# Kernel optimization log

Measured on AMD Instinct MI355X. Metric: run time of the kernel, lower is better.

## Reference

```python
import jax, jax.numpy as jnp
import numpy as np
import math

B, N, L = 1, 256, 384
D_MSA, D_PAIR, H, DH = 256, 128, 8, 32


def layer_norm(x, g, b, eps=1e-5):
    m = jnp.mean(x, axis=-1, keepdims=True)
    v = jnp.var(x, axis=-1, keepdims=True)
    return (x - m) * jax.lax.rsqrt(v + eps) * g + b


def setup_inputs() -> dict:
    key = jax.random.key(0)
    ks = jax.random.split(key, 16)
    hd = H * DH
    w = lambda k, shp, s=0.05: (jax.random.normal(k, shp, dtype=jnp.float32) * s)
    return {
        "msa": jax.random.normal(ks[0], (B, N, L, D_MSA), dtype=jnp.float32),
        "pair": jax.random.normal(ks[1], (B, L, L, D_PAIR), dtype=jnp.float32),
        "ln_msa_g": jnp.ones((D_MSA,), jnp.float32),
        "ln_msa_b": jnp.zeros((D_MSA,), jnp.float32),
        "ln_pair_g": jnp.ones((D_PAIR,), jnp.float32),
        "ln_pair_b": jnp.zeros((D_PAIR,), jnp.float32),
        "sw_q_w": w(ks[2], (D_MSA, hd)),
        "sw_q_b": jnp.zeros((hd,), jnp.float32),
        "sw_k_w": w(ks[3], (D_MSA, hd)),
        "sw_k_b": jnp.zeros((hd,), jnp.float32),
        "wq": w(ks[4], (D_MSA, hd)),
        "wk": w(ks[5], (D_MSA, hd)),
        "wv": w(ks[6], (D_MSA, hd)),
        "wb": w(ks[7], (D_PAIR, H)),
        "wg": w(ks[8], (D_MSA, hd)),
        "bg": jnp.ones((hd,), jnp.float32),
        "wo": w(ks[9], (hd, D_MSA)),
        "bo": jnp.zeros((D_MSA,), jnp.float32),
    }


def reference(msa, pair, ln_msa_g, ln_msa_b, ln_pair_g, ln_pair_b,
              sw_q_w, sw_q_b, sw_k_w, sw_k_b,
              wq, wk, wv, wb, wg, bg, wo, bo):
    b, n, l, _ = msa.shape
    scale = 1.0 / math.sqrt(DH)

    msa_n = layer_norm(msa, ln_msa_g, ln_msa_b)
    pair_n = layer_norm(pair, ln_pair_g, ln_pair_b)

    # SequenceWeight: attention of target seq (row 0) over all N rows, per (L, head)
    tar = msa_n[:, 0]                                       # [B,L,D]
    swq = (tar @ sw_q_w + sw_q_b).reshape(b, l, H, DH) * scale
    swk = (msa_n @ sw_k_w + sw_k_b).reshape(b, n, l, H, DH)
    sw_logits = jnp.einsum('blhd,bnlhd->bnlh', swq, swk)    # [B,N,L,H]
    seq_weight = jax.nn.softmax(sw_logits, axis=1)          # softmax over N (dropout: eval)

    query = (msa_n @ wq).reshape(b, n, l, H, DH) * seq_weight[..., None]
    key = (msa_n @ wk).reshape(b, n, l, H, DH) * scale
    value = (msa_n @ wv).reshape(b, n, l, H, DH)
    bias = pair_n @ wb                                      # [B,L,L,H]
    gate = jax.nn.sigmoid(msa_n @ wg + bg)                  # [B,N,L,H*DH]

    attn = jnp.einsum('bsqhd,bskhd->bqkh', query, key) + bias
    attn = jax.nn.softmax(attn, axis=-2)                    # over k axis
    out = jnp.einsum('bqkh,bskhd->bsqhd', attn, value).reshape(b, n, l, H * DH)
    out = gate * out
    return out @ wo + bo
```

## Files before the change

### kernel.cpp

```cpp
#include <hip/hip_runtime.h>
#include <hip/hip_fp16.h>
#include <stdint.h>

#define NSEQ 256
#define LSEQ 384
#define DM   256
#define DP   128
#define NH   8
#define DHD  32
#define NL   (NSEQ*LSEQ)
#define LL   (LSEQ*LSEQ)
#define SCALE 0.17677669529663687f

typedef unsigned short u16;
typedef short bf16x8 __attribute__((ext_vector_type(8)));
typedef float f32x4 __attribute__((ext_vector_type(4)));

__device__ __forceinline__ float b2f(u16 s){
  union { uint32_t u; float f; } v; v.u = ((uint32_t)s)<<16; return v.f;
}
__device__ __forceinline__ u16 f2b(float f){
  union { float f; uint32_t u; } v; v.f = f;
  uint32_t u = v.u;
  return (u16)((u + 0x7FFFu + ((u>>16)&1u)) >> 16);
}
__device__ __forceinline__ float wsum(float x){
  #pragma unroll
  for(int o=32;o>0;o>>=1) x += __shfl_xor(x,o,64);
  return x;
}
__device__ __forceinline__ float wmax(float x){
  #pragma unroll
  for(int o=32;o>0;o>>=1) x = fmaxf(x, __shfl_xor(x,o,64));
  return x;
}
__device__ __forceinline__ void gload16(const void* g, void* l){
  __builtin_amdgcn_global_load_lds((const __attribute__((address_space(1))) void*)g,
      (__attribute__((address_space(3))) void*)l, 16, 0, 0);
}

__global__ __launch_bounds__(256) void k_ln_msa(const float* __restrict__ msa,
    const float* __restrict__ g, const float* __restrict__ b, u16* __restrict__ out){
  int lane = threadIdx.x & 63;
  int64_t row = (int64_t)blockIdx.x*4 + (threadIdx.x>>6);
  const float4 x = *(const float4*)(msa + row*DM + lane*4);
  float s = x.x+x.y+x.z+x.w;
  float q = x.x*x.x+x.y*x.y+x.z*x.z+x.w*x.w;
  s = wsum(s); q = wsum(q);
  float mean = s*(1.0f/DM);
  float rstd = rsqrtf(q*(1.0f/DM) - mean*mean + 1e-5f);
  int c = lane*4;
  float4 gv = *(const float4*)(g+c);
  float4 bv = *(const float4*)(b+c);
  ushort4 o;
  o.x=f2b((x.x-mean)*rstd*gv.x+bv.x);
  o.y=f2b((x.y-mean)*rstd*gv.y+bv.y);
  o.z=f2b((x.z-mean)*rstd*gv.z+bv.z);
  o.w=f2b((x.w-mean)*rstd*gv.w+bv.w);
  *(ushort4*)(out + row*DM + c) = o;
}

__global__ __launch_bounds__(256) void k_wconv(const float* __restrict__ wq,
    const float* __restrict__ wk, const float* __restrict__ wv,
    const float* __restrict__ wg, const float* __restrict__ wo,
    u16* __restrict__ WTall, u16* __restrict__ WOT){
  __shared__ float tile[64][65];
  int z = blockIdx.z;
  const float* src = (z==0)?wq:(z==1)?wk:(z==2)?wv:(z==3)?wg:wo;
  u16* dst = (z<4) ? (WTall + z*DM*DM) : WOT;
  int k0 = blockIdx.x*64, n0 = blockIdx.y*64, t = threadIdx.x;
  int r = t>>4, c4 = (t&15)*4;
  #pragma unroll
  for(int it=0; it<4; it++){
    float4 v = *(const float4*)(src + (int64_t)(k0 + it*16 + r)*DM + n0 + c4);
    tile[it*16+r][c4+0]=v.x; tile[it*16+r][c4+1]=v.y;
    tile[it*16+r][c4+2]=v.z; tile[it*16+r][c4+3]=v.w;
  }
  __syncthreads();
  #pragma unroll
  for(int it=0; it<4; it++){
    int nl = it*16 + r, kl = c4;
    ushort4 o;
    o.x=f2b(tile[kl+0][nl]); o.y=f2b(tile[kl+1][nl]);
    o.z=f2b(tile[kl+2][nl]); o.w=f2b(tile[kl+3][nl]);
    *(ushort4*)(dst + (int64_t)(n0+nl)*DM + k0 + kl) = o;
  }
}

__global__ __launch_bounds__(256) void k_u(const u16* __restrict__ msa_n,
    const float* __restrict__ sw_q_w, const float* __restrict__ sw_q_b,
    const float* __restrict__ sw_k_w, float* __restrict__ u){
  __shared__ float tar[DM];
  __shared__ float swq[DM];
  int l = blockIdx.x, t = threadIdx.x;
  tar[t] = b2f(msa_n[(int64_t)l*DM + t]);
  __syncthreads();
  float acc = sw_q_b[t];
  for(int c=0;c<DM;c++) acc += tar[c]*sw_q_w[c*DM + t];
  swq[t] = acc * SCALE;
  __syncthreads();
  float res[NH];
  #pragma unroll
  for(int h=0;h<NH;h++){
    float a = 0.f;
    #pragma unroll
    for(int d=0;d<DHD;d+=4){
      float4 w = *(const float4*)(sw_k_w + t*DM + h*DHD + d);
      a += w.x*swq[h*DHD+d] + w.y*swq[h*DHD+d+1] + w.z*swq[h*DHD+d+2] + w.w*swq[h*DHD+d+3];
    }
    res[h]=a;
  }
  #pragma unroll
  for(int h=0;h<NH;h++) u[((int64_t)l*NH + h)*DM + t] = res[h];
}

__global__ __launch_bounds__(256) void k_seqw(const u16* __restrict__ msa_n,
    const float* __restrict__ u, float* __restrict__ sw){
  __shared__ float ul[NH*DM];
  __shared__ float lg[NH*256];
  __shared__ float mx[NH], sm[NH];
  int l = blockIdx.x, t = threadIdx.x;
  #pragma unroll
  for(int h=0;h<NH;h++) ul[h*DM+t] = u[((int64_t)l*NH+h)*DM + t];
  __syncthreads();
  float acc[NH] = {};
  const u16* row = msa_n + ((int64_t)t*LSEQ + l)*DM;
  for(int c=0;c<DM;c+=4){
    ushort4 xv = *(const ushort4*)(row + c);
    float x0=b2f(xv.x), x1=b2f(xv.y), x2=b2f(xv.z), x3=b2f(xv.w);
    #pragma unroll
    for(int h=0;h<NH;h++)
      acc[h] += x0*ul[h*DM+c] + x1*ul[h*DM+c+1] + x2*ul[h*DM+c+2] + x3*ul[h*DM+c+3];
  }
  #pragma unroll
  for(int h=0;h<NH;h++) lg[h*256+t] = acc[h];
  __syncthreads();
  int wv = t>>6, ln = t&63;
  for(int h=wv; h<NH; h+=4){
    float a=lg[h*256+ln], b=lg[h*256+ln+64], c=lg[h*256+ln+128], d=lg[h*256+ln+192];
    float m = wmax(fmaxf(fmaxf(a,b),fmaxf(c,d)));
    float e = __expf(a-m)+__expf(b-m)+__expf(c-m)+__expf(d-m);
    e = wsum(e);
    if(ln==0){ mx[h]=m; sm[h]=1.f/e; }
  }
  __syncthreads();
  float o[NH];
  #pragma unroll
  for(int h=0;h<NH;h++) o[h] = __expf(acc[h]-mx[h])*sm[h];
  float* dst = sw + ((int64_t)t*LSEQ + l)*NH;
  *(float4*)dst     = make_float4(o[0],o[1],o[2],o[3]);
  *(float4*)(dst+4) = make_float4(o[4],o[5],o[6],o[7]);
}

__global__ __launch_bounds__(256) void k_bias(const float* __restrict__ pair,
    const float* __restrict__ g, const float* __restrict__ b,
    const float* __restrict__ wb, float* __restrict__ bias){
  int64_t row = (int64_t)blockIdx.x*256 + threadIdx.x;
  const float* pr = pair + row*DP;
  uint2 xs[32];
  float s = 0.f, q = 0.f;
  #pragma unroll
  for(int i=0;i<32;i++){
    float4 v = *(const float4*)(pr + i*4);
    s += v.x+v.y+v.z+v.w;
    q += v.x*v.x+v.y*v.y+v.z*v.z+v.w*v.w;
    __half2 p0 = __floats2half2_rn(v.x, v.y);
    __half2 p1 = __floats2half2_rn(v.z, v.w);
    xs[i].x = *(const uint32_t*)&p0;
    xs[i].y = *(const uint32_t*)&p1;
  }
  float mean = s*(1.f/DP);
  float rstd = rsqrtf(q*(1.f/DP) - mean*mean + 1e-5f);
  float acc[NH] = {};
  #pragma unroll
  for(int i=0;i<32;i++){
    __half2 p0 = *(const __half2*)&xs[i].x;
    __half2 p1 = *(const __half2*)&xs[i].y;
    float2 f0 = __half22float2(p0);
    float2 f1 = __half22float2(p1);
    float xv[4] = {f0.x, f0.y, f1.x, f1.y};
    #pragma unroll
    for(int c4=0;c4<4;c4++){
      int c = i*4 + c4;
      float y = (xv[c4]-mean)*rstd*g[c] + b[c];
      #pragma unroll
      for(int h=0;h<NH;h++) acc[h] += y*wb[c*NH+h];
    }
  }
  #pragma unroll
  for(int h=0;h<NH;h++) bias[(int64_t)h*LL + row] = acc[h];
}


__global__ __launch_bounds__(256) void k_projf(const u16* __restrict__ A,
    const u16* __restrict__ WT, u16* __restrict__ qb, u16* __restrict__ kb,
    u16* __restrict__ gbuf, u16* __restrict__ VT,
    const float* __restrict__ sw, const float* __restrict__ bg){
  __shared__ short As[128*256];
  int t = threadIdx.x;
  int w = t>>6, lane = t&63, ln15 = lane&15, quad = lane>>4;
  int mw = (w>>1)*64, nw = (w&1)*64;
  int bx = blockIdx.x;
  int64_t r0 = (int64_t)bx*128;

  {
    int rowl = lane>>5;
    int pc = lane&31;
    #pragma unroll
    for(int m=0;m<16;m++){
      int q = w*16+m;
      int row = 2*q + rowl;
      int gch = pc ^ (row&7);
      gload16(A + (r0+row)*DM + gch*8, &As[q*512]);
    }
  }
  __syncthreads();

  for(int nt=0; nt<8; nt++){
    int n0 = nt*128;
    f32x4 acc[4][4] = {};
    #pragma unroll
    for(int ks=0; ks<8; ks++){
      bf16x8 af[4], bfv[4];
      #pragma unroll
      for(int j=0;j<4;j++)
        bfv[j] = *(const bf16x8*)(WT + (int64_t)(n0+nw+j*16+ln15)*DM + ks*32 + quad*8);
      #pragma unroll
      for(int i=0;i<4;i++){
        int row = mw+i*16+ln15;
        af[i] = *(const bf16x8*)&As[row*256 + (((ks*4+quad) ^ (ln15&7)))*8];
      }
      #pragma unroll
      for(int i=0;i<4;i++)
        #pragma unroll
        for(int j=0;j<4;j++)
          acc[i][j] = __builtin_amdgcn_mfma_f32_16x16x32_bf16(af[i], bfv[j], acc[i][j], 0,0,0);
    }
    int mode = nt>>1;
    int cmb = (nt&1)*128 + nw;
    if(mode==2){
      int s = bx/3, kb3 = (bx%3)*128 + mw;
      #pragma unroll
      for(int j=0;j<4;j++){
        int cm = cmb + j*16 + ln15;
        int hh = cm>>5, d = cm&31;
        #pragma unroll
        for(int i=0;i<4;i++){
          int kpos0 = kb3 + i*16 + quad*4;
          ushort4 o;
          o.x=f2b(acc[i][j][0]); o.y=f2b(acc[i][j][1]);
          o.z=f2b(acc[i][j][2]); o.w=f2b(acc[i][j][3]);
          *(ushort4*)(VT + ((int64_t)(hh*NSEQ+s)*DHD + d)*LSEQ + kpos0) = o;
        }
      }
    } else {
      u16* dst = (mode==0)?qb:(mode==1)?kb:gbuf;
      float bgv[4];
      if(mode==3){
        #pragma unroll
        for(int j=0;j<4;j++) bgv[j] = bg[cmb + j*16 + ln15];
      }
      #pragma unroll
      for(int i=0;i<4;i++)
        #pragma unroll
        for(int reg=0;reg<4;reg++){
          int64_t rr = r0 + mw + i*16 + quad*4 + reg;
          #pragma unroll
          for(int j=0;j<4;j++){
            int cm = cmb + j*16 + ln15;
            float v = acc[i][j][reg];
            if(mode==0)      v *= sw[rr*NH + (cm>>5)];
            else if(mode==1) v *= SCALE;
            else             v = 1.f/(1.f+__expf(-(v+bgv[j])));
            dst[rr*DM + cm] = f2b(v);
          }
        }
    }
  }
}

__global__ __launch_bounds__(256) void k_scores(const u16* __restrict__ Q,
    const u16* __restrict__ K, float* __restrict__ scores){
  __shared__ short As[128*64];
  __shared__ short Bs[128*64];
  int t = threadIdx.x;
  int w = t>>6, lane = t&63, ln15 = lane&15, quad = lane>>4;
  int rIn = lane>>3, cch = lane&7;
  int mw = (w>>1)*64, nw = (w&1)*64;
  int q0 = blockIdx.x*128, k0t = blockIdx.y*128;
  int h = blockIdx.z>>2, sc = blockIdx.z&3;
  int g = cch ^ rIn;
  int s_off = g>>2, d16 = g&3;
  f32x4 acc[4][4] = {};
  for(int i2=0; i2<32; i2++){
    int sb = sc*64 + i2*2 + s_off;
    __syncthreads();
    #pragma unroll
    for(int ti=0; ti<4; ti++){
      int row = w*32 + ti*8 + rIn;
      gload16(Q + ((int64_t)sb*LSEQ + q0 + row)*DM + h*DHD + d16*8, &As[(w*32+ti*8)*64]);
      gload16(K + ((int64_t)sb*LSEQ + k0t + row)*DM + h*DHD + d16*8, &Bs[(w*32+ti*8)*64]);
    }
    __syncthreads();
    #pragma unroll
    for(int kk=0;kk<2;kk++){
      int p = (kk*4+quad) ^ (lane&7);
      bf16x8 af[4], bfv[4];
      #pragma unroll
      for(int i=0;i<4;i++) af[i]  = *(const bf16x8*)&As[(mw+i*16+ln15)*64 + p*8];
      #pragma unroll
      for(int j=0;j<4;j++) bfv[j] = *(const bf16x8*)&Bs[(nw+j*16+ln15)*64 + p*8];
      #pragma unroll
      for(int i=0;i<4;i++)
        #pragma unroll
        for(int j=0;j<4;j++)
          acc[i][j] = __builtin_amdgcn_mfma_f32_16x16x32_bf16(af[i], bfv[j], acc[i][j], 0,0,0);
    }
  }
  int64_t slab = (int64_t)sc*NH*LL;
  #pragma unroll
  for(int i=0;i<4;i++)
    #pragma unroll
    for(int reg=0;reg<4;reg++){
      int q = q0 + mw + i*16 + quad*4 + reg;
      float* rp = scores + slab + ((int64_t)h*LSEQ + q)*LSEQ + k0t + nw + ln15;
      #pragma unroll
      for(int j=0;j<4;j++) rp[j*16] = acc[i][j][reg];
    }
}

__global__ __launch_bounds__(128) void k_softmax(const float* __restrict__ scores,
    const float* __restrict__ bias, u16* __restrict__ Pb){
  int hq = blockIdx.x, t = threadIdx.x;
  int64_t base = (int64_t)hq*LSEQ;
  float v[3];
  #pragma unroll
  for(int i=0;i<3;i++){
    int k = t + i*128;
    float x = bias[base+k];
    x += scores[base+k];
    x += scores[(int64_t)1*NH*LL + base + k];
    x += scores[(int64_t)2*NH*LL + base + k];
    x += scores[(int64_t)3*NH*LL + base + k];
    v[i]=x;
  }
  __shared__ float red[2], red2[2];
  int wv=t>>6, ln=t&63;
  float m = fmaxf(fmaxf(v[0],v[1]),v[2]);
  m = wmax(m);
  if(ln==0) red[wv]=m;
  __syncthreads();
  m = fmaxf(red[0],red[1]);
  float e = __expf(v[0]-m)+__expf(v[1]-m)+__expf(v[2]-m);
  e = wsum(e);
  if(ln==0) red2[wv]=e;
  __syncthreads();
  float inv = 1.f/(red2[0]+red2[1]);
  #pragma unroll
  for(int i=0;i<3;i++) Pb[base + t + i*128] = f2b(__expf(v[i]-m)*inv);
}

__global__ __launch_bounds__(256) void k_pv(const u16* __restrict__ VT,
    const u16* __restrict__ Pb, const u16* __restrict__ gbuf,
    u16* __restrict__ attn){
  __shared__ short As[128*64];
  __shared__ short Bs[128*64];
  int t = threadIdx.x;
  int w = t>>6, lane = t&63, ln15 = lane&15, quad = lane>>4;
  int rIn = lane>>3, cch = lane&7;
  int mw = (w>>1)*64, nw = (w&1)*64;
  int mx = blockIdx.x, ny = blockIdx.y, h = blockIdx.z;
  int g = cch ^ rIn;
  f32x4 acc[4][4] = {};
  for(int it=0; it<6; it++){
    int k0 = it*64;
    __syncthreads();
    #pragma unroll
    for(int ti=0; ti<4; ti++){
      int row = w*32 + ti*8 + rIn;
      gload16(VT + ((int64_t)h*8192 + mx*128 + row)*LSEQ + k0 + g*8, &As[(w*32+ti*8)*64]);
      gload16(Pb + ((int64_t)h*LSEQ + ny*128 + row)*LSEQ + k0 + g*8, &Bs[(w*32+ti*8)*64]);
    }
    __syncthreads();
    #pragma unroll
    for(int kk=0;kk<2;kk++){
      int p = (kk*4+quad) ^ (lane&7);
      bf16x8 af[4], bfv[4];
      #pragma unroll
      for(int i=0;i<4;i++) af[i]  = *(const bf16x8*)&As[(mw+i*16+ln15)*64 + p*8];
      #pragma unroll
      for(int j=0;j<4;j++) bfv[j] = *(const bf16x8*)&Bs[(nw+j*16+ln15)*64 + p*8];
      #pragma unroll
      for(int i=0;i<4;i++)
        #pragma unroll
        for(int j=0;j<4;j++)
          acc[i][j] = __builtin_amdgcn_mfma_f32_16x16x32_bf16(af[i], bfv[j], acc[i][j], 0,0,0);
    }
  }
  #pragma unroll
  for(int i=0;i<4;i++){
    int m0 = mx*128 + mw + i*16 + quad*4;
    int s = m0>>5, d0 = m0&31;
    #pragma unroll
    for(int j=0;j<4;j++){
      int q = ny*128 + nw + j*16 + ln15;
      int64_t base = ((int64_t)s*LSEQ + q)*DM + h*DHD + d0;
      ushort4 gv = *(const ushort4*)(gbuf + base);
      ushort4 o;
      o.x = f2b(acc[i][j][0]*b2f(gv.x));
      o.y = f2b(acc[i][j][1]*b2f(gv.y));
      o.z = f2b(acc[i][j][2]*b2f(gv.z));
      o.w = f2b(acc[i][j][3]*b2f(gv.w));
      *(ushort4*)(attn + base) = o;
    }
  }
}

__global__ __launch_bounds__(256) void k_final(const u16* __restrict__ A,
    const u16* __restrict__ WOT, const float* __restrict__ bo,
    float* __restrict__ out){
  __shared__ short As[128*256];
  int t = threadIdx.x;
  int w = t>>6, lane = t&63, ln15 = lane&15, quad = lane>>4;
  int mw = (w>>1)*64, nw = (w&1)*64;
  int64_t r0 = (int64_t)blockIdx.x*128;

  {
    int rowl = lane>>5;
    int pc = lane&31;
    #pragma unroll
    for(int m=0;m<16;m++){
      int q = w*16+m;
      int row = 2*q + rowl;
      int gch = pc ^ (row&7);
      gload16(A + (r0+row)*DM + gch*8, &As[q*512]);
    }
  }
  __syncthreads();

  for(int nt=0; nt<2; nt++){
    int n0 = nt*128;
    f32x4 acc[4][4] = {};
    #pragma unroll
    for(int ks=0; ks<8; ks++){
      bf16x8 af[4], bfv[4];
      #pragma unroll
      for(int j=0;j<4;j++)
        bfv[j] = *(const bf16x8*)(WOT + (int64_t)(n0+nw+j*16+ln15)*DM + ks*32 + quad*8);
      #pragma unroll
      for(int i=0;i<4;i++){
        int row = mw+i*16+ln15;
        af[i] = *(const bf16x8*)&As[row*256 + (((ks*4+quad) ^ (ln15&7)))*8];
      }
      #pragma unroll
      for(int i=0;i<4;i++)
        #pragma unroll
        for(int j=0;j<4;j++)
          acc[i][j] = __builtin_amdgcn_mfma_f32_16x16x32_bf16(af[i], bfv[j], acc[i][j], 0,0,0);
    }
    float bv[4];
    #pragma unroll
    for(int j=0;j<4;j++) bv[j] = bo[n0 + nw + j*16 + ln15];
    #pragma unroll
    for(int i=0;i<4;i++)
      #pragma unroll
      for(int reg=0;reg<4;reg++){
        int64_t r = r0 + mw + i*16 + quad*4 + reg;
        float* rp = out + r*DM + n0 + nw + ln15;
        #pragma unroll
        for(int j=0;j<4;j++) rp[j*16] = acc[i][j][reg] + bv[j];
      }
  }
}

extern "C" void kernel_launch(void* const* d_in, const int* in_sizes, int n_in,
                              void* d_out, int out_size, void* d_ws, size_t ws_size,
                              hipStream_t stream){
  const float* msa    = (const float*)d_in[0];
  const float* pair   = (const float*)d_in[1];
  const float* lmg    = (const float*)d_in[2];
  const float* lmb    = (const float*)d_in[3];
  const float* lpg    = (const float*)d_in[4];
  const float* lpb    = (const float*)d_in[5];
  const float* sw_q_w = (const float*)d_in[6];
  const float* sw_q_b = (const float*)d_in[7];
  const float* sw_k_w = (const float*)d_in[8];
  const float* wq     = (const float*)d_in[10];
  const float* wk     = (const float*)d_in[11];
  const float* wv     = (const float*)d_in[12];
  const float* wb     = (const float*)d_in[13];
  const float* wg     = (const float*)d_in[14];
  const float* bg     = (const float*)d_in[15];
  const float* wo     = (const float*)d_in[16];
  const float* bo     = (const float*)d_in[17];
  float* out = (float*)d_out;

  u16* msa_n = (u16*)d_ws;
  u16* qb    = msa_n + (int64_t)NL*DM;
  u16* kb    = qb + (int64_t)NL*DM;
  u16* gbuf  = kb + (int64_t)NL*DM;
  u16* VT    = gbuf + (int64_t)NL*DM;
  u16* Pb    = VT + (int64_t)NL*DM;
  u16* WTall = Pb + (int64_t)NH*LSEQ*LSEQ;
  u16* WOT   = WTall + 1024*DM;
  float* u_buf = (float*)(WOT + DM*DM);
  float* sw  = u_buf + (int64_t)LSEQ*NH*DM;
  float* bias = sw + (int64_t)NL*NH;
  float* scores = bias + (int64_t)NH*LL;
  u16* attnout = msa_n;

  k_ln_msa<<<NL/4, 256, 0, stream>>>(msa, lmg, lmb, msa_n);
  k_wconv<<<dim3(4,4,5), 256, 0, stream>>>(wq, wk, wv, wg, wo, WTall, WOT);
  k_u<<<LSEQ, 256, 0, stream>>>(msa_n, sw_q_w, sw_q_b, sw_k_w, u_buf);
  k_seqw<<<LSEQ, 256, 0, stream>>>(msa_n, u_buf, sw);
  k_bias<<<LL/256, 256, 0, stream>>>(pair, lpg, lpb, wb, bias);
  k_projf<<<dim3(NL/128), 256, 0, stream>>>(msa_n, WTall, qb, kb, gbuf, VT, sw, bg);
  k_scores<<<dim3(3,3,32), 256, 0, stream>>>(qb, kb, scores);
  k_softmax<<<NH*LSEQ, 128, 0, stream>>>(scores, bias, Pb);
  k_pv<<<dim3(64,3,NH), 256, 0, stream>>>(VT, Pb, gbuf, attnout);
  k_final<<<dim3(NL/128), 256, 0, stream>>>(attnout, WOT, bo, out);
}
```

Measured before the change: 742.0 us.

## Stage weight tiles in LDS, halve row tile, swap MFMA operands in projections

The projection and output GEMM kernels now use 64-row A tiles with 128x128 weight tiles staged in shared memory, instead of reading weight fragments straight from global memory. The MFMA operands are swapped so each lane holds four consecutive output columns, which allows vectorized ushort4/float4 stores for q/k/gate and the output. LDS drops from 64KB to 64KB total split differently, and launch bounds request 2 blocks per CU with twice as many blocks. The trade-offs are more barriers per tile, weights reloaded for every smaller row tile, and the VT transpose stores turning into scalar 2-byte writes.

```diff
diff --git a/kernel.cpp b/kernel.cpp
--- a/kernel.cpp
+++ b/kernel.cpp
@@ -192,89 +192,105 @@
 }
 
 
-__global__ __launch_bounds__(256) void k_projf(const u16* __restrict__ A,
+__global__ __launch_bounds__(256,2) void k_projf(const u16* __restrict__ A,
     const u16* __restrict__ WT, u16* __restrict__ qb, u16* __restrict__ kb,
     u16* __restrict__ gbuf, u16* __restrict__ VT,
     const float* __restrict__ sw, const float* __restrict__ bg){
-  __shared__ short As[128*256];
+  __shared__ short As[64*256];
+  __shared__ short Bs[128*128];
   int t = threadIdx.x;
   int w = t>>6, lane = t&63, ln15 = lane&15, quad = lane>>4;
-  int mw = (w>>1)*64, nw = (w&1)*64;
+  int mw = (w>>1)*32, nw = (w&1)*64;
   int bx = blockIdx.x;
-  int64_t r0 = (int64_t)bx*128;
+  int64_t r0 = (int64_t)bx*64;
 
   {
     int rowl = lane>>5;
     int pc = lane&31;
     #pragma unroll
-    for(int m=0;m<16;m++){
-      int q = w*16+m;
+    for(int m=0;m<8;m++){
+      int q = w*8+m;
       int row = 2*q + rowl;
       int gch = pc ^ (row&7);
       gload16(A + (r0+row)*DM + gch*8, &As[q*512]);
     }
   }
-  __syncthreads();
 
   for(int nt=0; nt<8; nt++){
-    int n0 = nt*128;
-    f32x4 acc[4][4] = {};
-    #pragma unroll
-    for(int ks=0; ks<8; ks++){
-      bf16x8 af[4], bfv[4];
-      #pragma unroll
-      for(int j=0;j<4;j++)
-        bfv[j] = *(const bf16x8*)(WT + (int64_t)(n0+nw+j*16+ln15)*DM + ks*32 + quad*8);
-      #pragma unroll
-      for(int i=0;i<4;i++){
-        int row = mw+i*16+ln15;
-        af[i] = *(const bf16x8*)&As[row*256 + (((ks*4+quad) ^ (ln15&7)))*8];
+    f32x4 acc[4][2] = {};
+    #pragma unroll
+    for(int kh=0; kh<2; kh++){
+      __syncthreads();
+      {
+        int rowl4 = lane>>4;
+        int pc16 = lane&15;
+        #pragma unroll
+        for(int m=0;m<8;m++){
+          int q = w*8+m;
+          int row = q*4 + rowl4;
+          int gch = pc16 ^ (row&7);
+          gload16(WT + (int64_t)(nt*128+row)*DM + kh*128 + gch*8, &Bs[q*512]);
+        }
       }
-      #pragma unroll
-      for(int i=0;i<4;i++)
+      __syncthreads();
+      #pragma unroll
+      for(int ks2=0; ks2<4; ks2++){
+        bf16x8 af[2], bfv[4];
+        #pragma unroll
+        for(int i=0;i<2;i++){
+          int rw = mw+i*16+ln15;
+          int ca = (kh*16 + ks2*4 + quad) ^ (rw&7);
+          af[i] = *(const bf16x8*)&As[rw*256 + ca*8];
+        }
+        #pragma unroll
+        for(int j=0;j<4;j++){
+          int rw = nw+j*16+ln15;
+          int cb = (ks2*4+quad) ^ (rw&7);
+          bfv[j] = *(const bf16x8*)&Bs[rw*128 + cb*8];
+        }
         #pragma unroll
         for(int j=0;j<4;j++)
-          acc[i][j] = __builtin_amdgcn_mfma_f32_16x16x32_bf16(af[i], bfv[j], acc[i][j], 0,0,0);
+          #pragma unroll
+          for(int i=0;i<2;i++)
+            acc[j][i] = __builtin_amdgcn_mfma_f32_16x16x32_bf16(bfv[j], af[i], acc[j][i], 0,0,0);
+      }
     }
     int mode = nt>>1;
     int cmb = (nt&1)*128 + nw;
     if(mode==2){
-      int s = bx/3, kb3 = (bx%3)*128 + mw;
-      #pragma unroll
-      for(int j=0;j<4;j++){
-        int cm = cmb + j*16 + ln15;
-        int hh = cm>>5, d = cm&31;
-        #pragma unroll
-        for(int i=0;i<4;i++){
-          int kpos0 = kb3 + i*16 + quad*4;
-          ushort4 o;
-          o.x=f2b(acc[i][j][0]); o.y=f2b(acc[i][j][1]);
-          o.z=f2b(acc[i][j][2]); o.w=f2b(acc[i][j][3]);
-          *(ushort4*)(VT + ((int64_t)(hh*NSEQ+s)*DHD + d)*LSEQ + kpos0) = o;
-        }
-      }
+      int s = bx/6, kpb = (bx%6)*64 + mw;
+      #pragma unroll
+      for(int j=0;j<4;j++)
+        #pragma unroll
+        for(int i=0;i<2;i++){
+          int kpos = kpb + i*16 + ln15;
+          #pragma unroll
+          for(int reg=0;reg<4;reg++){
+            int cm = cmb + j*16 + quad*4 + reg;
+            int hh = cm>>5, d = cm&31;
+            VT[((int64_t)(hh*NSEQ+s)*DHD + d)*LSEQ + kpos] = f2b(acc[j][i][reg]);
+          }
+        }
     } else {
       u16* dst = (mode==0)?qb:(mode==1)?kb:gbuf;
-      float bgv[4];
-      if(mode==3){
-        #pragma unroll
-        for(int j=0;j<4;j++) bgv[j] = bg[cmb + j*16 + ln15];
+      #pragma unroll
+      for(int i=0;i<2;i++){
+        int64_t rr = r0 + mw + i*16 + ln15;
+        #pragma unroll
+        for(int j=0;j<4;j++){
+          int cm0 = cmb + j*16 + quad*4;
+          ushort4 o;
+          #pragma unroll
+          for(int reg=0;reg<4;reg++){
+            float v = acc[j][i][reg];
+            if(mode==0)      v *= sw[rr*NH + ((cm0+reg)>>5)];
+            else if(mode==1) v *= SCALE;
+            else             v = 1.f/(1.f+__expf(-(v+bg[cm0+reg])));
+            ((u16*)&o)[reg] = f2b(v);
+          }
+          *(ushort4*)(dst + rr*DM + cm0) = o;
+        }
       }
-      #pragma unroll
-      for(int i=0;i<4;i++)
-        #pragma unroll
-        for(int reg=0;reg<4;reg++){
-          int64_t rr = r0 + mw + i*16 + quad*4 + reg;
-          #pragma unroll
-          for(int j=0;j<4;j++){
-            int cm = cmb + j*16 + ln15;
-            float v = acc[i][j][reg];
-            if(mode==0)      v *= sw[rr*NH + (cm>>5)];
-            else if(mode==1) v *= SCALE;
-            else             v = 1.f/(1.f+__expf(-(v+bgv[j])));
-            dst[rr*DM + cm] = f2b(v);
-          }
-        }
     }
   }
 }
@@ -416,60 +432,82 @@
   }
 }
 
-__global__ __launch_bounds__(256) void k_final(const u16* __restrict__ A,
+__global__ __launch_bounds__(256,2) void k_final(const u16* __restrict__ A,
     const u16* __restrict__ WOT, const float* __restrict__ bo,
     float* __restrict__ out){
-  __shared__ short As[128*256];
+  __shared__ short As[64*256];
+  __shared__ short Bs[128*128];
   int t = threadIdx.x;
   int w = t>>6, lane = t&63, ln15 = lane&15, quad = lane>>4;
-  int mw = (w>>1)*64, nw = (w&1)*64;
-  int64_t r0 = (int64_t)blockIdx.x*128;
+  int mw = (w>>1)*32, nw = (w&1)*64;
+  int64_t r0 = (int64_t)blockIdx.x*64;
 
   {
     int rowl = lane>>5;
     int pc = lane&31;
     #pragma unroll
-    for(int m=0;m<16;m++){
-      int q = w*16+m;
+    for(int m=0;m<8;m++){
+      int q = w*8+m;
       int row = 2*q + rowl;
       int gch = pc ^ (row&7);
       gload16(A + (r0+row)*DM + gch*8, &As[q*512]);
     }
   }
-  __syncthreads();
 
   for(int nt=0; nt<2; nt++){
+    f32x4 acc[4][2] = {};
+    #pragma unroll
+    for(int kh=0; kh<2; kh++){
+      __syncthreads();
+      {
+        int rowl4 = lane>>4;
+        int pc16 = lane&15;
+        #pragma unroll
+        for(int m=0;m<8;m++){
+          int q = w*8+m;
+          int row = q*4 + rowl4;
+          int gch = pc16 ^ (row&7);
+          gload16(WOT + (int64_t)(nt*128+row)*DM + kh*128 + gch*8, &Bs[q*512]);
+        }
+      }
+      __syncthreads();
+      #pragma unroll
+      for(int ks2=0; ks2<4; ks2++){
+        bf16x8 af[2], bfv[4];
+        #pragma unroll
+        for(int i=0;i<2;i++){
+          int rw = mw+i*16+ln15;
+          int ca = (kh*16 + ks2*4 + quad) ^ (rw&7);
+          af[i] = *(const bf16x8*)&As[rw*256 + ca*8];
+        }
+        #pragma unroll
+        for(int j=0;j<4;j++){
+          int rw = nw+j*16+ln15;
+          int cb = (ks2*4+quad) ^ (rw&7);
+          bfv[j] = *(const bf16x8*)&Bs[rw*128 + cb*8];
+        }
+        #pragma unroll
+        for(int j=0;j<4;j++)
+          #pragma unroll
+          for(int i=0;i<2;i++)
+            acc[j][i] = __builtin_amdgcn_mfma_f32_16x16x32_bf16(bfv[j], af[i], acc[j][i], 0,0,0);
+      }
+    }
     int n0 = nt*128;
-    f32x4 acc[4][4] = {};
-    #pragma unroll
-    for(int ks=0; ks<8; ks++){
-      bf16x8 af[4], bfv[4];
-      #pragma unroll
-      for(int j=0;j<4;j++)
-        bfv[j] = *(const bf16x8*)(WOT + (int64_t)(n0+nw+j*16+ln15)*DM + ks*32 + quad*8);
-      #pragma unroll
-      for(int i=0;i<4;i++){
-        int row = mw+i*16+ln15;
-        af[i] = *(const bf16x8*)&As[row*256 + (((ks*4+quad) ^ (ln15&7)))*8];
+    #pragma unroll
+    for(int i=0;i<2;i++){
+      int64_t rr = r0 + mw + i*16 + ln15;
+      #pragma unroll
+      for(int j=0;j<4;j++){
+        int cm0 = n0 + nw + j*16 + quad*4;
+        float4 o;
+        o.x = acc[j][i][0] + bo[cm0+0];
+        o.y = acc[j][i][1] + bo[cm0+1];
+        o.z = acc[j][i][2] + bo[cm0+2];
+        o.w = acc[j][i][3] + bo[cm0+3];
+        *(float4*)(out + rr*DM + cm0) = o;
       }
-      #pragma unroll
-      for(int i=0;i<4;i++)
-        #pragma unroll
-        for(int j=0;j<4;j++)
-          acc[i][j] = __builtin_amdgcn_mfma_f32_16x16x32_bf16(af[i], bfv[j], acc[i][j], 0,0,0);
-    }
-    float bv[4];
-    #pragma unroll
-    for(int j=0;j<4;j++) bv[j] = bo[n0 + nw + j*16 + ln15];
-    #pragma unroll
-    for(int i=0;i<4;i++)
-      #pragma unroll
-      for(int reg=0;reg<4;reg++){
-        int64_t r = r0 + mw + i*16 + quad*4 + reg;
-        float* rp = out + r*DM + n0 + nw + ln15;
-        #pragma unroll
-        for(int j=0;j<4;j++) rp[j*16] = acc[i][j][reg] + bv[j];
-      }
+    }
   }
 }
 
@@ -514,9 +552,9 @@
   k_u<<<LSEQ, 256, 0, stream>>>(msa_n, sw_q_w, sw_q_b, sw_k_w, u_buf);
   k_seqw<<<LSEQ, 256, 0, stream>>>(msa_n, u_buf, sw);
   k_bias<<<LL/256, 256, 0, stream>>>(pair, lpg, lpb, wb, bias);
-  k_projf<<<dim3(NL/128), 256, 0, stream>>>(msa_n, WTall, qb, kb, gbuf, VT, sw, bg);
+  k_projf<<<dim3(NL/64), 256, 0, stream>>>(msa_n, WTall, qb, kb, gbuf, VT, sw, bg);
   k_scores<<<dim3(3,3,32), 256, 0, stream>>>(qb, kb, scores);
   k_softmax<<<NH*LSEQ, 128, 0, stream>>>(scores, bias, Pb);
   k_pv<<<dim3(64,3,NH), 256, 0, stream>>>(VT, Pb, gbuf, attnout);
-  k_final<<<dim3(NL/128), 256, 0, stream>>>(attnout, WOT, bo, out);
-}
+  k_final<<<dim3(NL/64), 256, 0, stream>>>(attnout, WOT, bo, out);
+}
```

New measurement: 683.0 us. -8.0%, faster.
